# Kernel tuning notes

Measured on AMD Instinct MI355X. Metric: run time of the kernel, lower is better.

The kernel has to match this reference:

```python
import jax, jax.numpy as jnp
import numpy as np


def setup_inputs() -> dict:
    key = jax.random.key(0)
    k1, k2 = jax.random.split(key)
    node_num = 10000
    n_edges = 640000
    d = 128
    embs = jax.random.normal(k1, (node_num, d), dtype=jnp.float32)
    ratings = jax.random.randint(k2, (n_edges, 2), 0, node_num, dtype=jnp.int32)
    return {"embs": embs, "ratings": ratings, "node_num": node_num}


def reference(embs, ratings, node_num):
    # edge endpoints: row (source) and column (neighbor) indices
    r0 = ratings[:, 0]
    r1 = ratings[:, 1]
    # edge dot-product attention scores  [E]
    scores = jnp.sum(embs[r0] * embs[r1], axis=-1)
    # sparse row-wise softmax (torch.sparse.softmax over dim=1)
    seg_max = jax.ops.segment_max(scores, r0, num_segments=node_num)
    seg_max = jnp.where(jnp.isfinite(seg_max), seg_max, jnp.float32(0.0))  # empty rows
    ex = jnp.exp(scores - seg_max[r0])
    denom = jax.ops.segment_sum(ex, r0, num_segments=node_num)
    attn = ex / denom[r0]
    # attention weights are detached in the original module
    attn = jax.lax.stop_gradient(attn)
    # sparse mm aggregation: out[i] = sum_{e: r0[e]=i} attn[e] * embs[r1[e]]
    out = jax.ops.segment_sum(attn[:, None] * embs[r1], r0, num_segments=node_num)
    return out
```

## Files before the change

### kernel.cpp

```cpp
#include <hip/hip_runtime.h>
#include <hip/hip_bf16.h>
#include <math.h>


#define K_CHUNKS 256
#define NODE_LDS 10240
#define NPAD 10240
#define STAGE_LDS 2560
#define EXP_CLAMP 80.0f
#define MAXE 192

__global__ __launch_bounds__(1024) void build_kernel(const int2* __restrict__ ratings,
                             unsigned short* __restrict__ mtmp,
                             unsigned short* __restrict__ staging,
                             int n_edges, int node_num, int chunk_size) {
    __shared__ int hist[NODE_LDS];
    __shared__ unsigned short stage[STAGE_LDS];
    __shared__ int lds_ws[16];
    __shared__ int lds_wp[16];

    int tid  = threadIdx.x;
    int lane = tid & 63;
    int wid  = tid >> 6;
    int k    = blockIdx.x;

    for (int i = tid; i < NODE_LDS; i += 1024) hist[i] = 0;
    __syncthreads();

    int base = k * chunk_size;
    int end  = base + chunk_size; if (end > n_edges) end = n_edges;

    for (int e = base + tid; e < end; e += 1024)
        atomicAdd(&hist[ratings[e].x], 1);
    __syncthreads();

    const int B = NODE_LDS / 1024;
    int b0 = tid * B;
    int c[B];
    int local = 0;
    #pragma unroll
    for (int j = 0; j < B; ++j) {
        c[j] = hist[b0 + j];
        local += c[j];
    }
    int incl = local;
    #pragma unroll
    for (int off = 1; off < 64; off <<= 1) {
        int t = __shfl_up(incl, off, 64);
        if (lane >= off) incl += t;
    }
    if (lane == 63) lds_ws[wid] = incl;
    __syncthreads();
    if (wid == 0 && lane < 16) {
        int wv = lds_ws[lane];
        #pragma unroll
        for (int off = 1; off < 16; off <<= 1) {
            int t = __shfl_up(wv, off, 64);
            if (lane >= off) wv += t;
        }
        lds_wp[lane] = wv;
    }
    __syncthreads();
    int run = ((wid > 0) ? lds_wp[wid - 1] : 0) + (incl - local);

    unsigned short* mrow = mtmp + (size_t)k * NPAD;
    #pragma unroll
    for (int j = 0; j < B; ++j) {
        int i = b0 + j;
        int cc = (c[j] > 15) ? 15 : c[j];
        mrow[i] = (unsigned short)(((unsigned int)run << 4) | (unsigned int)cc);
        hist[i] = run;
        run += c[j];
    }
    __syncthreads();

    for (int e = base + tid; e < end; e += 1024) {
        int2 r = ratings[e];
        int pos = atomicAdd(&hist[r.x], 1);
        if (pos < STAGE_LDS) stage[pos] = (unsigned short)r.y;
    }
    __syncthreads();

    int nsh = end - base;
    unsigned int* g  = (unsigned int*)(staging + (size_t)k * chunk_size);
    unsigned int* sg = (unsigned int*)stage;
    int nu = (nsh + 1) >> 1;
    for (int i = tid; i < nu; i += 1024) g[i] = sg[i];
}

__global__ __launch_bounds__(256) void transpose_kernel(const unsigned short* __restrict__ mtmp,
                                                        unsigned short* __restrict__ meta_t,
                                                        int node_num) {
    __shared__ unsigned short tile[64][66];
    int n0 = blockIdx.x * 64;
    int k0 = blockIdx.y * 64;
    int tx = threadIdx.x & 63;
    int ty = threadIdx.x >> 6;
    #pragma unroll
    for (int r = 0; r < 64; r += 4) {
        int n = n0 + tx;
        tile[r + ty][tx] = (n < node_num) ? mtmp[(size_t)(k0 + r + ty) * NPAD + n] : 0;
    }
    __syncthreads();
    #pragma unroll
    for (int r = 0; r < 64; r += 4) {
        int n = n0 + r + ty;
        if (n < node_num)
            meta_t[(size_t)n * K_CHUNKS + k0 + tx] = tile[tx][r + ty];
    }
}

__global__ __launch_bounds__(256) void node_kernel(const float* __restrict__ embs,
                            const unsigned short* __restrict__ meta_t,
                            const unsigned short* __restrict__ staging,
                            float* __restrict__ out,
                            int node_num, int chunk_size) {
    __shared__ int s_r1[4][MAXE];

    int tid   = threadIdx.x;
    int lane  = tid & 63;
    int wslot = tid >> 6;
    int g     = lane >> 4;
    int t     = lane & 15;
    int n     = blockIdx.x * 4 + wslot;
    bool nvalid = (n < node_num);
    int nc    = nvalid ? n : 0;

    const uint2* mrow = (const uint2*)(meta_t + (size_t)nc * K_CHUNKS);
    uint2 mm = nvalid ? mrow[lane] : make_uint2(0u, 0u);
    unsigned int mw[4] = { mm.x & 0xffffu, mm.x >> 16, mm.y & 0xffffu, mm.y >> 16 };
    int cj[4], oj[4];
    int cnt = 0;
    #pragma unroll
    for (int j = 0; j < 4; ++j) {
        cj[j] = (int)(mw[j] & 15u);
        oj[j] = (int)(mw[j] >> 4);
        cnt += cj[j];
    }
    int incl = cnt;
    #pragma unroll
    for (int off = 1; off < 64; off <<= 1) {
        int tt = __shfl_up(incl, off, 64);
        if (lane >= off) incl += tt;
    }
    int basep = incl - cnt;
    int E = __shfl(incl, 63, 64);
    if (E > MAXE) E = MAXE;
    {
        int idx = basep;
        #pragma unroll
        for (int j = 0; j < 4; ++j) {
            const unsigned short* s0 = staging + (size_t)(lane * 4 + j) * chunk_size + oj[j];
            for (int q = 0; q < cj[j]; ++q) {
                if (idx < MAXE) s_r1[wslot][idx] = (int)s0[q];
                ++idx;
            }
        }
    }
    __syncthreads();

    const float4* row_n = (const float4*)(embs + (size_t)nc * 128);
    float4 av0 = row_n[t];
    float4 av1 = row_n[16 + t];

    float  l = 0.f;
    float4 acc0 = make_float4(0.f, 0.f, 0.f, 0.f);
    float4 acc1 = make_float4(0.f, 0.f, 0.f, 0.f);

    if (!nvalid) return;

    for (int base = 0; base < E; base += 16) {
        bool  valid[4];
        int   r1[4];
        #pragma unroll
        for (int b = 0; b < 4; ++b) {
            int idx = base + b * 4 + g;
            valid[b] = (idx < E);
            r1[b] = valid[b] ? s_r1[wslot][idx] : 0;
        }
        float4 v0[4], v1[4];
        #pragma unroll
        for (int b = 0; b < 4; ++b) {
            const float4* row = (const float4*)(embs + (size_t)r1[b] * 128);
            v0[b] = row[t];
            v1[b] = row[16 + t];
        }
        float s[4];
        #pragma unroll
        for (int b = 0; b < 4; ++b) {
            float d = v0[b].x * av0.x;
            d = fmaf(v0[b].y, av0.y, d);
            d = fmaf(v0[b].z, av0.z, d);
            d = fmaf(v0[b].w, av0.w, d);
            d = fmaf(v1[b].x, av1.x, d);
            d = fmaf(v1[b].y, av1.y, d);
            d = fmaf(v1[b].z, av1.z, d);
            d = fmaf(v1[b].w, av1.w, d);
            s[b] = d;
        }
        #pragma unroll
        for (int b = 0; b < 4; ++b) {
            #pragma unroll
            for (int off = 1; off < 16; off <<= 1)
                s[b] += __shfl_xor(s[b], off, 64);
        }
        float p[4];
        #pragma unroll
        for (int b = 0; b < 4; ++b)
            p[b] = valid[b] ? __expf(fminf(s[b], EXP_CLAMP)) : 0.f;
        l += (p[0] + p[1]) + (p[2] + p[3]);
        #pragma unroll
        for (int b = 0; b < 4; ++b) {
            acc0.x = fmaf(p[b], v0[b].x, acc0.x);
            acc0.y = fmaf(p[b], v0[b].y, acc0.y);
            acc0.z = fmaf(p[b], v0[b].z, acc0.z);
            acc0.w = fmaf(p[b], v0[b].w, acc0.w);
            acc1.x = fmaf(p[b], v1[b].x, acc1.x);
            acc1.y = fmaf(p[b], v1[b].y, acc1.y);
            acc1.z = fmaf(p[b], v1[b].z, acc1.z);
            acc1.w = fmaf(p[b], v1[b].w, acc1.w);
        }
    }

    #pragma unroll
    for (int off = 16; off <= 32; off <<= 1) {
        l      += __shfl_xor(l,      off, 64);
        acc0.x += __shfl_xor(acc0.x, off, 64);
        acc0.y += __shfl_xor(acc0.y, off, 64);
        acc0.z += __shfl_xor(acc0.z, off, 64);
        acc0.w += __shfl_xor(acc0.w, off, 64);
        acc1.x += __shfl_xor(acc1.x, off, 64);
        acc1.y += __shfl_xor(acc1.y, off, 64);
        acc1.z += __shfl_xor(acc1.z, off, 64);
        acc1.w += __shfl_xor(acc1.w, off, 64);
    }

    float inv = (l > 0.f) ? 1.f / l : 0.f;
    if (g == 0) {
        float4* orow = (float4*)(out + (size_t)n * 128);
        orow[t]      = make_float4(acc0.x * inv, acc0.y * inv, acc0.z * inv, acc0.w * inv);
        orow[16 + t] = make_float4(acc1.x * inv, acc1.y * inv, acc1.z * inv, acc1.w * inv);
    }
}

extern "C" void kernel_launch(void* const* d_in, const int* in_sizes, int n_in,
                              void* d_out, int out_size, void* d_ws, size_t ws_size,
                              hipStream_t stream) {
    const float* embs    = (const float*)d_in[0];
    const int*   ratings = (const int*)d_in[1];
    const int d        = 128;
    const int node_num = in_sizes[0] / d;
    const int n_edges  = in_sizes[1] / 2;
    float* out = (float*)d_out;

    int chunk_size = (n_edges + K_CHUNKS - 1) / K_CHUNKS;
    if (chunk_size & 1) chunk_size += 1;

    auto align256 = [](size_t x) { return (x + 255) & ~(size_t)255; };
    char* ws = (char*)d_ws;
    unsigned short* mtmp = (unsigned short*)ws;
    ws += align256((size_t)K_CHUNKS * NPAD * 2);
    unsigned short* meta_t = (unsigned short*)ws;
    ws += align256((size_t)node_num * K_CHUNKS * 2);
    unsigned short* staging = (unsigned short*)ws;
    ws += align256((size_t)K_CHUNKS * chunk_size * 2);

    build_kernel<<<K_CHUNKS, 1024, 0, stream>>>(
        (const int2*)ratings, mtmp, staging, n_edges, node_num, chunk_size);

    {
        dim3 grid((node_num + 63) / 64, K_CHUNKS / 64);
        transpose_kernel<<<grid, 256, 0, stream>>>(mtmp, meta_t, node_num);
    }

    {
        int blocks = (node_num + 3) / 4;
        node_kernel<<<blocks, 256, 0, stream>>>(embs, meta_t, staging, out, node_num, chunk_size);
    }
}
```

Measured before the change: 101.0 us.

## Split each node's edge list across two waves and merge partials via LDS

Each node is now processed by two wavefronts, each handling half of the chunk metadata and its own edge list, instead of a single wave per node. Partial accumulators and softmax denominators from the second wave are passed through shared memory and combined by the first wave before writing. This shortens the per-node serial gather loop and raises the number of waves in flight, at the cost of duplicated per-wave setup (own row load, scan) and an added block barrier.

```diff
diff --git a/kernel.cpp b/kernel.cpp
--- a/kernel.cpp
+++ b/kernel.cpp
@@ -8,7 +8,7 @@
 #define NPAD 10240
 #define STAGE_LDS 2560
 #define EXP_CLAMP 80.0f
-#define MAXE 192
+#define MAXE_W 128
 
 __global__ __launch_bounds__(1024) void build_kernel(const int2* __restrict__ ratings,
                              unsigned short* __restrict__ mtmp,
@@ -115,28 +115,27 @@
                             const unsigned short* __restrict__ staging,
                             float* __restrict__ out,
                             int node_num, int chunk_size) {
-    __shared__ int s_r1[4][MAXE];
+    __shared__ int    s_r1[4][MAXE_W];
+    __shared__ float4 s_acc[2][2][16];
+    __shared__ float  s_l[2];
 
     int tid   = threadIdx.x;
     int lane  = tid & 63;
-    int wslot = tid >> 6;
+    int wid   = tid >> 6;
+    int slot  = wid >> 1;
+    int w     = wid & 1;
     int g     = lane >> 4;
     int t     = lane & 15;
-    int n     = blockIdx.x * 4 + wslot;
+    int n     = blockIdx.x * 2 + slot;
     bool nvalid = (n < node_num);
     int nc    = nvalid ? n : 0;
 
-    const uint2* mrow = (const uint2*)(meta_t + (size_t)nc * K_CHUNKS);
-    uint2 mm = nvalid ? mrow[lane] : make_uint2(0u, 0u);
-    unsigned int mw[4] = { mm.x & 0xffffu, mm.x >> 16, mm.y & 0xffffu, mm.y >> 16 };
-    int cj[4], oj[4];
-    int cnt = 0;
-    #pragma unroll
-    for (int j = 0; j < 4; ++j) {
-        cj[j] = (int)(mw[j] & 15u);
-        oj[j] = (int)(mw[j] >> 4);
-        cnt += cj[j];
-    }
+    const unsigned int* mrow32 = (const unsigned int*)(meta_t + (size_t)nc * K_CHUNKS);
+    unsigned int mm = nvalid ? mrow32[w * 64 + lane] : 0u;
+    unsigned int e0 = mm & 0xffffu, e1 = mm >> 16;
+    int c0 = (int)(e0 & 15u), o0 = (int)(e0 >> 4);
+    int c1 = (int)(e1 & 15u), o1 = (int)(e1 >> 4);
+    int cnt = c0 + c1;
     int incl = cnt;
     #pragma unroll
     for (int off = 1; off < 64; off <<= 1) {
@@ -145,19 +144,21 @@
     }
     int basep = incl - cnt;
     int E = __shfl(incl, 63, 64);
-    if (E > MAXE) E = MAXE;
+    if (E > MAXE_W) E = MAXE_W;
     {
+        int k0 = w * 128 + lane * 2;
         int idx = basep;
-        #pragma unroll
-        for (int j = 0; j < 4; ++j) {
-            const unsigned short* s0 = staging + (size_t)(lane * 4 + j) * chunk_size + oj[j];
-            for (int q = 0; q < cj[j]; ++q) {
-                if (idx < MAXE) s_r1[wslot][idx] = (int)s0[q];
-                ++idx;
-            }
-        }
-    }
-    __syncthreads();
+        const unsigned short* s0 = staging + (size_t)k0 * chunk_size + o0;
+        for (int q = 0; q < c0; ++q) {
+            if (idx < MAXE_W) s_r1[wid][idx] = (int)s0[q];
+            ++idx;
+        }
+        const unsigned short* s1 = staging + (size_t)(k0 + 1) * chunk_size + o1;
+        for (int q = 0; q < c1; ++q) {
+            if (idx < MAXE_W) s_r1[wid][idx] = (int)s1[q];
+            ++idx;
+        }
+    }
 
     const float4* row_n = (const float4*)(embs + (size_t)nc * 128);
     float4 av0 = row_n[t];
@@ -167,8 +168,6 @@
     float4 acc0 = make_float4(0.f, 0.f, 0.f, 0.f);
     float4 acc1 = make_float4(0.f, 0.f, 0.f, 0.f);
 
-    if (!nvalid) return;
-
     for (int base = 0; base < E; base += 16) {
         bool  valid[4];
         int   r1[4];
@@ -176,7 +175,7 @@
         for (int b = 0; b < 4; ++b) {
             int idx = base + b * 4 + g;
             valid[b] = (idx < E);
-            r1[b] = valid[b] ? s_r1[wslot][idx] : 0;
+            r1[b] = valid[b] ? s_r1[wid][idx] : 0;
         }
         float4 v0[4], v1[4];
         #pragma unroll
@@ -235,11 +234,22 @@
         acc1.w += __shfl_xor(acc1.w, off, 64);
     }
 
-    float inv = (l > 0.f) ? 1.f / l : 0.f;
-    if (g == 0) {
+    if (w == 1 && g == 0) {
+        s_acc[slot][0][t] = acc0;
+        s_acc[slot][1][t] = acc1;
+        if (lane == 0) s_l[slot] = l;
+    }
+    __syncthreads();
+    if (w == 0 && g == 0 && nvalid) {
+        float4 b0 = s_acc[slot][0][t];
+        float4 b1 = s_acc[slot][1][t];
+        float L = l + s_l[slot];
+        float inv = (L > 0.f) ? 1.f / L : 0.f;
         float4* orow = (float4*)(out + (size_t)n * 128);
-        orow[t]      = make_float4(acc0.x * inv, acc0.y * inv, acc0.z * inv, acc0.w * inv);
-        orow[16 + t] = make_float4(acc1.x * inv, acc1.y * inv, acc1.z * inv, acc1.w * inv);
+        orow[t]      = make_float4((acc0.x + b0.x) * inv, (acc0.y + b0.y) * inv,
+                                   (acc0.z + b0.z) * inv, (acc0.w + b0.w) * inv);
+        orow[16 + t] = make_float4((acc1.x + b1.x) * inv, (acc1.y + b1.y) * inv,
+                                   (acc1.z + b1.z) * inv, (acc1.w + b1.w) * inv);
     }
 }
 
@@ -274,7 +284,7 @@
     }
 
     {
-        int blocks = (node_num + 3) / 4;
+        int blocks = (node_num + 1) / 2;
         node_kernel<<<blocks, 256, 0, stream>>>(embs, meta_t, staging, out, node_num, chunk_size);
     }
 }
```

After: 101.0 us. Within noise of the previous version (-0.0%).
